# Kernel tuning notes

Hardware: AMD Instinct MI355X
Metric: run time of the kernel (lower is better)

Reference implementation:

```python
import jax, jax.numpy as jnp
import numpy as np

B = 256      # batch
C = 512      # num_classes (independent heads)
F = 768      # BERT pooler_output dim (hard-coded in module)
D = 512      # dense_layer_size


def setup_inputs() -> dict:
    key = jax.random.key(0)
    ks = jax.random.split(key, 7)
    s1 = 1.0 / np.sqrt(F)
    s2 = 1.0 / np.sqrt(D)
    return {
        "x":  jax.random.normal(ks[0], (B, F), dtype=jnp.float32),
        "W1": jax.random.normal(ks[1], (C, F, D), dtype=jnp.float32) * s1,
        "b1": jax.random.normal(ks[2], (C, D), dtype=jnp.float32) * s1,
        "W2": jax.random.normal(ks[3], (C, D, D), dtype=jnp.float32) * s2,
        "b2": jax.random.normal(ks[4], (C, D), dtype=jnp.float32) * s2,
        "W3": jax.random.normal(ks[5], (C, D, 2), dtype=jnp.float32) * s2,
        "b3": jax.random.normal(ks[6], (C, 2), dtype=jnp.float32) * s2,
    }


def reference(x, W1, b1, W2, b2, W3, b3):
    # Batched version of the per-class Python loop:
    # each head: Linear(F,D)-ReLU-(Dropout=identity in eval)-Linear(D,D)-ReLU-Linear(D,2)
    h = jax.nn.relu(jnp.einsum('bf,cfd->bcd', x, W1) + b1[None])        # [B, C, D]
    h = jax.nn.relu(jnp.einsum('bcd,cde->bce', h, W2) + b2[None])        # [B, C, D]
    out = jnp.einsum('bcd,cde->bce', h, W3) + b3[None]                   # [B, C, 2]
    return out
```

## Files before the change

kernel.cpp:

```cpp
#include <hip/hip_runtime.h>
#include <stdint.h>

typedef float f32x4 __attribute__((ext_vector_type(4)));
typedef float f32x2 __attribute__((ext_vector_type(2)));
typedef short bf16x8 __attribute__((ext_vector_type(8)));
typedef uint32_t u32x4 __attribute__((ext_vector_type(4)));

__device__ __forceinline__ uint32_t bf16_rne(float f) {
  uint32_t x = __float_as_uint(f);
  return (x + 0x7FFFu + ((x >> 16) & 1u)) >> 16;
}

__device__ __forceinline__ void ldsbar() {
  asm volatile("s_waitcnt lgkmcnt(0)\n\ts_barrier" ::: "memory");
}

__global__ void cast_x_kernel(const float* __restrict__ x,
                              uint32_t* __restrict__ xb, int n2) {
  int i = blockIdx.x * 256 + threadIdx.x;
  if (i >= n2) return;
  f32x2 v = *(const f32x2*)(x + 2 * i);
  xb[i] = bf16_rne(v[0]) | (bf16_rne(v[1]) << 16);
}

template <int K, int MODE>
__global__ __launch_bounds__(512, 4) void gemm_fused(
    const uint16_t* __restrict__ Abase, long long aClassStride,
    const float* __restrict__ Wbase, const float* __restrict__ biasBase,
    uint16_t* __restrict__ Hout, const float* __restrict__ W3base,
    float* __restrict__ part) {
  constexpr int NT = K / 64;
  __shared__ uint8_t smem[16384];

  const int tid = threadIdx.x;
  const int bid = blockIdx.x;
  const int logical = ((bid & 7) << 9) | (bid >> 3);
  const int c = logical >> 3;
  const int nt = logical & 7;
  const int n0 = nt * 64;

  const uint16_t* Ab = Abase + (size_t)c * (size_t)aClassStride;
  const float* Wc = Wbase + (size_t)c * (K * 512) + n0;

  const int l = tid & 63, w = tid >> 6;
  const int lr = l & 15, lg = l >> 4;

  const uint16_t* Ap = Ab + (size_t)(w * 32 + lr) * K + lg * 8;

  f32x4 acc[2][4];
#pragma unroll
  for (int i = 0; i < 2; i++)
#pragma unroll
    for (int j = 0; j < 4; j++) acc[i][j] = {0.f, 0.f, 0.f, 0.f};

  auto loadB = [&](int ts, float* g) {
    const float* Ws = Wc + (size_t)(ts * 64 + w * 8) * 512 + l;
#pragma unroll
    for (int r = 0; r < 8; r++) g[r] = Ws[(size_t)r * 512];
  };
  auto writeB = [&](const float* g, int buf) {
    u32x4 p;
#pragma unroll
    for (int j = 0; j < 4; j++)
      p[j] = bf16_rne(g[2 * j]) | (bf16_rne(g[2 * j + 1]) << 16);
    *(u32x4*)(smem + buf * 8192 + l * 128 + ((w ^ (l & 7)) << 4)) = p;
  };
  auto comp = [&](int buf, int t) {
    const uint8_t* s = smem + buf * 8192;
    bf16x8 a[4];
#pragma unroll
    for (int kk = 0; kk < 2; ++kk)
#pragma unroll
      for (int mf = 0; mf < 2; mf++)
        a[kk * 2 + mf] =
            *(const bf16x8*)(Ap + t * 64 + kk * 32 + (size_t)mf * 16 * K);
#pragma unroll
    for (int kk = 0; kk < 2; ++kk) {
      const int kx = ((lg * 16) ^ ((lr & 7) << 4)) ^ (kk << 6);
      bf16x8 b[4];
#pragma unroll
      for (int nf = 0; nf < 4; nf++)
        b[nf] = *(const bf16x8*)(s + (nf * 16 + lr) * 128 + kx);
#pragma unroll
      for (int mf = 0; mf < 2; mf++)
#pragma unroll
        for (int nf = 0; nf < 4; nf++)
          acc[mf][nf] = __builtin_amdgcn_mfma_f32_16x16x32_bf16(
              a[kk * 2 + mf], b[nf], acc[mf][nf], 0, 0, 0);
    }
  };

  float g0[8], g1[8];
  loadB(0, g0);
  loadB(1, g1);
  writeB(g0, 0);
  ldsbar();

#pragma unroll 1
  for (int t = 0; t < NT; t += 2) {
    comp(0, t);
    if (t + 2 < NT) loadB(t + 2, g0);
    writeB(g1, 1);
    ldsbar();
    comp(1, t + 1);
    if (t + 3 < NT) loadB(t + 3, g1);
    if (t + 2 < NT) {
      writeB(g0, 0);
      ldsbar();
    }
  }

  float bv[4];
#pragma unroll
  for (int nf = 0; nf < 4; nf++)
    bv[nf] = biasBase[c * 512 + n0 + nf * 16 + lr];

  if constexpr (MODE == 0) {
    uint16_t* Oc = Hout + (size_t)c * 131072 + n0;
#pragma unroll
    for (int mf = 0; mf < 2; mf++)
#pragma unroll
      for (int nf = 0; nf < 4; nf++)
#pragma unroll
        for (int r = 0; r < 4; r++) {
          int m = w * 32 + mf * 16 + lg * 4 + r;
          float v = fmaxf(acc[mf][nf][r] + bv[nf], 0.f);
          Oc[(size_t)m * 512 + nf * 16 + lr] = (uint16_t)bf16_rne(v);
        }
  } else {
    float w30[4], w31[4];
#pragma unroll
    for (int nf = 0; nf < 4; nf++) {
      f32x2 t = *(const f32x2*)(W3base +
                                ((size_t)c * 512 + n0 + nf * 16 + lr) * 2);
      w30[nf] = t[0];
      w31[nf] = t[1];
    }
#pragma unroll
    for (int mf = 0; mf < 2; mf++)
#pragma unroll
      for (int r = 0; r < 4; r++) {
        float s0 = 0.f, s1 = 0.f;
#pragma unroll
        for (int nf = 0; nf < 4; nf++) {
          float v = fmaxf(acc[mf][nf][r] + bv[nf], 0.f);
          s0 += v * w30[nf];
          s1 += v * w31[nf];
        }
#pragma unroll
        for (int d = 1; d < 16; d <<= 1) {
          s0 += __shfl_xor(s0, d);
          s1 += __shfl_xor(s1, d);
        }
        if (lr == 0) {
          int m = w * 32 + mf * 16 + lg * 4 + r;
          *(f32x2*)(part + (((size_t)c * 256 + m) * 8 + nt) * 2) =
              f32x2{s0, s1};
        }
      }
  }
}

__global__ __launch_bounds__(512) void reduce_out(
    const float* __restrict__ part, const float* __restrict__ b3,
    float* __restrict__ out) {
  const int b = blockIdx.x, c = threadIdx.x;
  const f32x4* p = (const f32x4*)(part + ((size_t)c * 256 + b) * 16);
  f32x4 v0 = p[0], v1 = p[1], v2 = p[2], v3 = p[3];
  float s0 = b3[c * 2] + v0[0] + v0[2] + v1[0] + v1[2] + v2[0] + v2[2] +
             v3[0] + v3[2];
  float s1 = b3[c * 2 + 1] + v0[1] + v0[3] + v1[1] + v1[3] + v2[1] + v2[3] +
             v3[1] + v3[3];
  *(f32x2*)(out + ((size_t)b * 512 + c) * 2) = f32x2{s0, s1};
}

extern "C" void kernel_launch(void* const* d_in, const int* in_sizes, int n_in,
                              void* d_out, int out_size, void* d_ws,
                              size_t ws_size, hipStream_t stream) {
  const float* x = (const float*)d_in[0];
  const float* W1 = (const float*)d_in[1];
  const float* b1 = (const float*)d_in[2];
  const float* W2 = (const float*)d_in[3];
  const float* b2 = (const float*)d_in[4];
  const float* W3 = (const float*)d_in[5];
  const float* b3 = (const float*)d_in[6];
  float* out = (float*)d_out;

  uint8_t* ws = (uint8_t*)d_ws;
  const size_t xb_off = 0;
  const size_t h1_off = 393216;
  const size_t part_off = h1_off + 134217728;
  const size_t need = part_off + 8388608;
  if (ws_size < need) return;

  uint32_t* xb = (uint32_t*)(ws + xb_off);
  uint16_t* h1 = (uint16_t*)(ws + h1_off);
  float* part = (float*)(ws + part_off);

  cast_x_kernel<<<dim3(384), dim3(256), 0, stream>>>(x, xb, 98304);
  gemm_fused<768, 0><<<dim3(4096), dim3(512), 0, stream>>>(
      (const uint16_t*)xb, 0LL, W1, b1, h1, nullptr, nullptr);
  gemm_fused<512, 1><<<dim3(4096), dim3(512), 0, stream>>>(
      h1, 131072LL, W2, b2, nullptr, W3, part);
  reduce_out<<<dim3(256), dim3(512), 0, stream>>>(part, b3, out);
}
```

Measured before the change: 482.5 us.

## Fuse both MLP layers and the output head into one kernel, keeping h1 in LDS

Replaces the two per-layer GEMM launches and the reduction kernel with one fused kernel. Each block owns one class and half of the batch. It computes layer 1 into a swizzled bf16 h1 tile held in LDS, then computes layer 2 from LDS and folds the W3 projection and b3 into the epilogue, writing output directly. This removes the global h1 round trip, the partial-sum buffer and two launches. In exchange each class's fp32 weights are streamed by two blocks instead of one, relying on cache reuse between them. The large LDS footprint also limits occupancy to one block per CU, and the B pipeline is deepened to four register stages to compensate.

```diff
diff --git a/kernel.cpp b/kernel.cpp
--- a/kernel.cpp
+++ b/kernel.cpp
@@ -23,40 +23,47 @@
   xb[i] = bf16_rne(v[0]) | (bf16_rne(v[1]) << 16);
 }
 
-template <int K, int MODE>
-__global__ __launch_bounds__(512, 4) void gemm_fused(
-    const uint16_t* __restrict__ Abase, long long aClassStride,
-    const float* __restrict__ Wbase, const float* __restrict__ biasBase,
-    uint16_t* __restrict__ Hout, const float* __restrict__ W3base,
-    float* __restrict__ part) {
-  constexpr int NT = K / 64;
-  __shared__ uint8_t smem[16384];
+__global__ __launch_bounds__(512, 2) void fused_mlp(
+    const uint16_t* __restrict__ xb, const float* __restrict__ W1,
+    const float* __restrict__ b1, const float* __restrict__ W2,
+    const float* __restrict__ b2, const float* __restrict__ W3,
+    const float* __restrict__ b3, float* __restrict__ out) {
+  constexpr int H1OFF = 28672;
+  __shared__ uint8_t smem[159744];
 
   const int tid = threadIdx.x;
   const int bid = blockIdx.x;
-  const int logical = ((bid & 7) << 9) | (bid >> 3);
-  const int c = logical >> 3;
-  const int nt = logical & 7;
-  const int n0 = nt * 64;
-
-  const uint16_t* Ab = Abase + (size_t)c * (size_t)aClassStride;
-  const float* Wc = Wbase + (size_t)c * (K * 512) + n0;
+  const int logical = ((bid & 7) << 7) | (bid >> 3);
+  const int c = logical >> 1;
+  const int mh = logical & 1;
+
+  const float* W1c = W1 + (size_t)c * (768 * 512);
+  const float* W2c = W2 + (size_t)c * (512 * 512);
 
   const int l = tid & 63, w = tid >> 6;
   const int lr = l & 15, lg = l >> 4;
 
-  const uint16_t* Ap = Ab + (size_t)(w * 32 + lr) * K + lg * 8;
-
-  f32x4 acc[2][4];
-#pragma unroll
-  for (int i = 0; i < 2; i++)
-#pragma unroll
-    for (int j = 0; j < 4; j++) acc[i][j] = {0.f, 0.f, 0.f, 0.f};
-
-  auto loadB = [&](int ts, float* g) {
-    const float* Ws = Wc + (size_t)(ts * 64 + w * 8) * 512 + l;
-#pragma unroll
-    for (int r = 0; r < 8; r++) g[r] = Ws[(size_t)r * 512];
+  ((float*)(smem + 16384))[tid] = b1[(size_t)c * 512 + tid];
+  ((float*)(smem + 18432))[tid] = b2[(size_t)c * 512 + tid];
+  ((float*)(smem + 20480))[tid] = W3[(size_t)c * 1024 + tid];
+  ((float*)(smem + 20480))[tid + 512] = W3[(size_t)c * 1024 + 512 + tid];
+  if (tid < 2) ((float*)(smem + 24576))[tid] = b3[c * 2 + tid];
+
+  const uint16_t* Ap1 = xb + (size_t)(mh * 128 + w * 16 + lr) * 768 + lg * 8;
+  const int h1rd = H1OFF + (w * 16 + lr) * 1024;
+
+  f32x4 acc[4];
+#pragma unroll
+  for (int j = 0; j < 4; j++) acc[j] = {0.f, 0.f, 0.f, 0.f};
+
+  auto loadB = [&](const float* Wc, int nts, int ts, float* g) {
+    const float* p = Wc + (size_t)(ts * 64 + w * 8) * 512 + nts * 64 + l;
+#pragma unroll
+    for (int r = 0; r < 8; r++) g[r] = p[(size_t)r * 512];
+  };
+  auto loadA1 = [&](int ts, bf16x8* a2) {
+    a2[0] = *(const bf16x8*)(Ap1 + ts * 64);
+    a2[1] = *(const bf16x8*)(Ap1 + ts * 64 + 32);
   };
   auto writeB = [&](const float* g, int buf) {
     u32x4 p;
@@ -65,113 +72,136 @@
       p[j] = bf16_rne(g[2 * j]) | (bf16_rne(g[2 * j + 1]) << 16);
     *(u32x4*)(smem + buf * 8192 + l * 128 + ((w ^ (l & 7)) << 4)) = p;
   };
-  auto comp = [&](int buf, int t) {
+  auto compB = [&](int buf, int kk) {
     const uint8_t* s = smem + buf * 8192;
-    bf16x8 a[4];
-#pragma unroll
-    for (int kk = 0; kk < 2; ++kk)
-#pragma unroll
-      for (int mf = 0; mf < 2; mf++)
-        a[kk * 2 + mf] =
-            *(const bf16x8*)(Ap + t * 64 + kk * 32 + (size_t)mf * 16 * K);
+    const int kx = ((lg * 16) ^ ((lr & 7) << 4)) ^ (kk << 6);
+    bf16x8 b0 = *(const bf16x8*)(s + (0 * 16 + lr) * 128 + kx);
+    bf16x8 b1f = *(const bf16x8*)(s + (1 * 16 + lr) * 128 + kx);
+    bf16x8 b2f = *(const bf16x8*)(s + (2 * 16 + lr) * 128 + kx);
+    bf16x8 b3f = *(const bf16x8*)(s + (3 * 16 + lr) * 128 + kx);
+    struct { bf16x8 b[4]; } r = {{b0, b1f, b2f, b3f}};
+    return r;
+  };
+  auto comp1 = [&](int buf, const bf16x8* a2) {
 #pragma unroll
     for (int kk = 0; kk < 2; ++kk) {
-      const int kx = ((lg * 16) ^ ((lr & 7) << 4)) ^ (kk << 6);
-      bf16x8 b[4];
+      auto bb = compB(buf, kk);
 #pragma unroll
       for (int nf = 0; nf < 4; nf++)
-        b[nf] = *(const bf16x8*)(s + (nf * 16 + lr) * 128 + kx);
-#pragma unroll
-      for (int mf = 0; mf < 2; mf++)
-#pragma unroll
-        for (int nf = 0; nf < 4; nf++)
-          acc[mf][nf] = __builtin_amdgcn_mfma_f32_16x16x32_bf16(
-              a[kk * 2 + mf], b[nf], acc[mf][nf], 0, 0, 0);
-    }
-  };
-
-  float g0[8], g1[8];
-  loadB(0, g0);
-  loadB(1, g1);
-  writeB(g0, 0);
+        acc[nf] = __builtin_amdgcn_mfma_f32_16x16x32_bf16(a2[kk], bb.b[nf],
+                                                          acc[nf], 0, 0, 0);
+    }
+  };
+  auto comp2 = [&](int buf, int ts) {
+#pragma unroll
+    for (int kk = 0; kk < 2; ++kk) {
+      bf16x8 av = *(const bf16x8*)(
+          smem + h1rd + ((ts * 8 + ((kk * 4 + lg) ^ (lr & 7))) << 4));
+      auto bb = compB(buf, kk);
+#pragma unroll
+      for (int nf = 0; nf < 4; nf++)
+        acc[nf] = __builtin_amdgcn_mfma_f32_16x16x32_bf16(av, bb.b[nf],
+                                                          acc[nf], 0, 0, 0);
+    }
+  };
+
+  float g[4][8];
+  bf16x8 a[2][2];
+
+  loadB(W1c, 0, 0, g[0]);
+  loadB(W1c, 0, 1, g[1]);
+  loadA1(0, a[0]);
+  loadB(W1c, 0, 2, g[2]);
+  loadA1(1, a[1]);
+  loadB(W1c, 0, 3, g[3]);
+  writeB(g[0], 0);
   ldsbar();
 
 #pragma unroll 1
-  for (int t = 0; t < NT; t += 2) {
-    comp(0, t);
-    if (t + 2 < NT) loadB(t + 2, g0);
-    writeB(g1, 1);
-    ldsbar();
-    comp(1, t + 1);
-    if (t + 3 < NT) loadB(t + 3, g1);
-    if (t + 2 < NT) {
-      writeB(g0, 0);
-      ldsbar();
+  for (int so = 0; so < 8; ++so) {
+#pragma unroll
+    for (int k = 0; k < 12; ++k) {
+      comp1(k & 1, a[k & 1]);
+      if (k == 11) {
+        const int n0 = so * 64;
+#pragma unroll
+        for (int nf = 0; nf < 4; nf++) {
+          float bv = ((const float*)(smem + 16384))[n0 + nf * 16 + lr];
+#pragma unroll
+          for (int r = 0; r < 4; r++) {
+            int row = w * 16 + lg * 4 + r;
+            int ch = so * 8 + nf * 2 + (lr >> 3);
+            float v = fmaxf(acc[nf][r] + bv, 0.f);
+            *(uint16_t*)(smem + H1OFF + row * 1024 +
+                         ((ch ^ (row & 7)) << 4) + (lr & 7) * 2) =
+                (uint16_t)bf16_rne(v);
+          }
+          acc[nf] = {0.f, 0.f, 0.f, 0.f};
+        }
+      }
+      const bool last = (so == 7 && k == 11);
+      if (!last) writeB(g[(k + 1) & 3], (k + 1) & 1);
+      if (!(so == 7 && k >= 10)) loadA1((k + 2) % 12, a[k & 1]);
+      if (!(so == 7 && k >= 8)) {
+        int k4 = k + 4;
+        loadB(W1c, so + (k4 >= 12), k4 >= 12 ? k4 - 12 : k4, g[k & 3]);
+      }
+      if (!last) ldsbar();
     }
   }
 
-  float bv[4];
-#pragma unroll
-  for (int nf = 0; nf < 4; nf++)
-    bv[nf] = biasBase[c * 512 + n0 + nf * 16 + lr];
-
-  if constexpr (MODE == 0) {
-    uint16_t* Oc = Hout + (size_t)c * 131072 + n0;
-#pragma unroll
-    for (int mf = 0; mf < 2; mf++)
-#pragma unroll
-      for (int nf = 0; nf < 4; nf++)
-#pragma unroll
-        for (int r = 0; r < 4; r++) {
-          int m = w * 32 + mf * 16 + lg * 4 + r;
-          float v = fmaxf(acc[mf][nf][r] + bv[nf], 0.f);
-          Oc[(size_t)m * 512 + nf * 16 + lr] = (uint16_t)bf16_rne(v);
+  float s0[4] = {0.f, 0.f, 0.f, 0.f}, s1[4] = {0.f, 0.f, 0.f, 0.f};
+  loadB(W2c, 0, 0, g[0]);
+  loadB(W2c, 0, 1, g[1]);
+  loadB(W2c, 0, 2, g[2]);
+  loadB(W2c, 0, 3, g[3]);
+  writeB(g[0], 0);
+  ldsbar();
+
+#pragma unroll 1
+  for (int so = 0; so < 8; ++so) {
+#pragma unroll
+    for (int k = 0; k < 8; ++k) {
+      comp2(k & 1, k);
+      if (k == 7) {
+        const int n0 = so * 64;
+#pragma unroll
+        for (int nf = 0; nf < 4; nf++) {
+          float bv = ((const float*)(smem + 18432))[n0 + nf * 16 + lr];
+          f32x2 w3p = ((const f32x2*)(smem + 20480))[n0 + nf * 16 + lr];
+#pragma unroll
+          for (int r = 0; r < 4; r++) {
+            float v = fmaxf(acc[nf][r] + bv, 0.f);
+            s0[r] += v * w3p[0];
+            s1[r] += v * w3p[1];
+          }
+          acc[nf] = {0.f, 0.f, 0.f, 0.f};
         }
-  } else {
-    float w30[4], w31[4];
-#pragma unroll
-    for (int nf = 0; nf < 4; nf++) {
-      f32x2 t = *(const f32x2*)(W3base +
-                                ((size_t)c * 512 + n0 + nf * 16 + lr) * 2);
-      w30[nf] = t[0];
-      w31[nf] = t[1];
-    }
-#pragma unroll
-    for (int mf = 0; mf < 2; mf++)
-#pragma unroll
-      for (int r = 0; r < 4; r++) {
-        float s0 = 0.f, s1 = 0.f;
-#pragma unroll
-        for (int nf = 0; nf < 4; nf++) {
-          float v = fmaxf(acc[mf][nf][r] + bv[nf], 0.f);
-          s0 += v * w30[nf];
-          s1 += v * w31[nf];
-        }
-#pragma unroll
-        for (int d = 1; d < 16; d <<= 1) {
-          s0 += __shfl_xor(s0, d);
-          s1 += __shfl_xor(s1, d);
-        }
-        if (lr == 0) {
-          int m = w * 32 + mf * 16 + lg * 4 + r;
-          *(f32x2*)(part + (((size_t)c * 256 + m) * 8 + nt) * 2) =
-              f32x2{s0, s1};
-        }
-      }
+      }
+      const bool last = (so == 7 && k == 7);
+      if (!last) writeB(g[(k + 1) & 3], (k + 1) & 1);
+      if (!(so == 7 && k >= 4)) {
+        int k4 = k + 4;
+        loadB(W2c, so + (k4 >= 8 ? 1 : 0), k4 & 7, g[k & 3]);
+      }
+      if (!last) ldsbar();
+    }
   }
-}
-
-__global__ __launch_bounds__(512) void reduce_out(
-    const float* __restrict__ part, const float* __restrict__ b3,
-    float* __restrict__ out) {
-  const int b = blockIdx.x, c = threadIdx.x;
-  const f32x4* p = (const f32x4*)(part + ((size_t)c * 256 + b) * 16);
-  f32x4 v0 = p[0], v1 = p[1], v2 = p[2], v3 = p[3];
-  float s0 = b3[c * 2] + v0[0] + v0[2] + v1[0] + v1[2] + v2[0] + v2[2] +
-             v3[0] + v3[2];
-  float s1 = b3[c * 2 + 1] + v0[1] + v0[3] + v1[1] + v1[3] + v2[1] + v2[3] +
-             v3[1] + v3[3];
-  *(f32x2*)(out + ((size_t)b * 512 + c) * 2) = f32x2{s0, s1};
+
+  f32x2 b3v = *(const f32x2*)(smem + 24576);
+#pragma unroll
+  for (int r = 0; r < 4; r++) {
+#pragma unroll
+    for (int d = 1; d < 16; d <<= 1) {
+      s0[r] += __shfl_xor(s0[r], d);
+      s1[r] += __shfl_xor(s1[r], d);
+    }
+    if (lr == 0) {
+      int row = mh * 128 + w * 16 + lg * 4 + r;
+      *(f32x2*)(out + ((size_t)row * 512 + c) * 2) =
+          f32x2{s0[r] + b3v[0], s1[r] + b3v[1]};
+    }
+  }
 }
 
 extern "C" void kernel_launch(void* const* d_in, const int* in_sizes, int n_in,
@@ -187,20 +217,10 @@
   float* out = (float*)d_out;
 
   uint8_t* ws = (uint8_t*)d_ws;
-  const size_t xb_off = 0;
-  const size_t h1_off = 393216;
-  const size_t part_off = h1_off + 134217728;
-  const size_t need = part_off + 8388608;
-  if (ws_size < need) return;
-
-  uint32_t* xb = (uint32_t*)(ws + xb_off);
-  uint16_t* h1 = (uint16_t*)(ws + h1_off);
-  float* part = (float*)(ws + part_off);
+  if (ws_size < 393216) return;
+  uint32_t* xb = (uint32_t*)ws;
 
   cast_x_kernel<<<dim3(384), dim3(256), 0, stream>>>(x, xb, 98304);
-  gemm_fused<768, 0><<<dim3(4096), dim3(512), 0, stream>>>(
-      (const uint16_t*)xb, 0LL, W1, b1, h1, nullptr, nullptr);
-  gemm_fused<512, 1><<<dim3(4096), dim3(512), 0, stream>>>(
-      h1, 131072LL, W2, b2, nullptr, W3, part);
-  reduce_out<<<dim3(256), dim3(512), 0, stream>>>(part, b3, out);
-}
+  fused_mlp<<<dim3(1024), dim3(512), 0, stream>>>(
+      (const uint16_t*)xb, W1, b1, W2, b2, W3, b3, out);
+}
```

After: 410.9 us. -14.8%, faster.
